# Optimization experiments

Measured on AMD Instinct MI355X. Metric: run time of the kernel, lower is better.

The kernel has to match this reference:

```python
import jax, jax.numpy as jnp
import numpy as np

D = 1024      # d_model
H = 16        # num_heads
HW = D // H   # head_width = 64
FF = 4 * D    # hidden_dim = 4096
BATCH = 2
T = 2048
EPS = 1e-5


def layer_norm(x, g, b):
    mu = jnp.mean(x, axis=-1, keepdims=True)
    var = jnp.mean(jnp.square(x - mu), axis=-1, keepdims=True)
    return (x - mu) * jax.lax.rsqrt(var + EPS) * g + b


def setup_inputs() -> dict:
    key = jax.random.key(0)
    ks = jax.random.split(key, 7)
    s = 0.02
    return {
        "x": jax.random.normal(ks[0], (BATCH, T, D), dtype=jnp.float32),
        "Wq": jax.random.normal(ks[1], (D, D), dtype=jnp.float32) * s,
        "Wk": jax.random.normal(ks[2], (D, D), dtype=jnp.float32) * s,
        "Wv": jax.random.normal(ks[3], (D, D), dtype=jnp.float32) * s,
        "W1": jax.random.normal(ks[4], (FF, D), dtype=jnp.float32) * s,
        "W2": jax.random.normal(ks[5], (D, FF), dtype=jnp.float32) * s,
        "g1": jnp.ones((D,), dtype=jnp.float32),
        "b1": jnp.zeros((D,), dtype=jnp.float32),
        "g2": jnp.ones((D,), dtype=jnp.float32),
        "b2": jnp.zeros((D,), dtype=jnp.float32),
    }


def reference(x, Wq, Wk, Wv, W1, W2, g1, b1, g2, b2):
    N, t, d = x.shape
    # norm1
    xn = layer_norm(x, g1, b1)

    # --- MHSA with ALiBi + causal mask (math mirrors torch module) ---
    def heads(y):  # (N,t,D) -> (N,H,t,HW)
        return y.reshape(N, t, H, HW).transpose(0, 2, 1, 3)

    q = heads(xn @ Wq.T)
    k = heads(xn @ Wk.T)
    v = heads(xn @ Wv.T)

    scores = jnp.einsum("nhqd,nhkd->nhqk", q, k) / np.sqrt(HW).astype(np.float32)

    pos = jnp.arange(t)
    rel = (pos[None, :] - pos[:, None]).astype(x.dtype)           # [t,t], rel[i,j]=j-i
    slopes = (2.0 ** (-(jnp.arange(1, H + 1)) * (8.0 / H))).astype(x.dtype)  # [H]
    alibi = slopes[:, None, None] * rel                            # [H,t,t]
    causal = jnp.where(pos[None, :] > pos[:, None],
                       jnp.array(-jnp.inf, x.dtype),
                       jnp.array(0.0, x.dtype))                    # [t,t]

    att = jax.nn.softmax(scores + alibi[None] + causal[None, None], axis=-1)
    o = jnp.einsum("nhqk,nhkd->nhqd", att, v)
    o = o.transpose(0, 2, 1, 3).reshape(N, t, d)

    att_out = xn + o

    # --- MLP: Linear -> SiLU -> Linear ---
    h = layer_norm(att_out, g2, b2)
    m = jax.nn.silu(h @ W1.T) @ W2.T
    return att_out + m
```

## Files before the change

### kernel.cpp

```cpp
#include <hip/hip_runtime.h>

#define DMODEL 1024
#define NHEAD  16
#define HWID   64
#define FFDIM  4096
#define NBATCH 2
#define SEQT   2048
#define NTOK   4096
#define QKLD   3072

using bf8    = __attribute__((ext_vector_type(8))) short;
using f32x4  = __attribute__((ext_vector_type(4))) float;
using f32x16 = __attribute__((ext_vector_type(16))) float;

__device__ inline short to_bf16(float f) {
  unsigned u = __float_as_uint(f);
  return (short)((u + 0x7fffu + ((u >> 16) & 1u)) >> 16);
}
__device__ inline float from_bf16(short s) {
  return __uint_as_float(((unsigned)(unsigned short)s) << 16);
}
__device__ inline float exp2_fast(float x) {
  float r;
  asm("v_exp_f32 %0, %1" : "=v"(r) : "v"(x));
  return r;
}
__device__ inline unsigned cvt_pk_bf16(float lo, float hi) {
  unsigned r;
  asm("v_cvt_pk_bf16_f32 %0, %1, %2" : "=v"(r) : "v"(lo), "v"(hi));
  return r;
}
__device__ inline void lds_load16(const void* g, void* l) {
  __builtin_amdgcn_global_load_lds(
      (const __attribute__((address_space(1))) void*)g,
      (__attribute__((address_space(3))) void*)l, 16, 0, 0);
}

__global__ __launch_bounds__(256)
void cvt_kernel(const float* __restrict__ in, short* __restrict__ out, int n4) {
  int i = blockIdx.x * 256 + threadIdx.x;
  if (i < n4) {
    float4 v = ((const float4*)in)[i];
    short4 o;
    o.x = to_bf16(v.x); o.y = to_bf16(v.y);
    o.z = to_bf16(v.z); o.w = to_bf16(v.w);
    ((short4*)out)[i] = o;
  }
}

__global__ __launch_bounds__(256)
void ln_kernel(const float* __restrict__ x, const float* __restrict__ g,
               const float* __restrict__ b, short* __restrict__ out) {
  const int row = blockIdx.x;
  const int t = threadIdx.x;
  const float4 v = ((const float4*)(x + (long)row * DMODEL))[t];
  float s  = v.x + v.y + v.z + v.w;
  float s2 = v.x * v.x + v.y * v.y + v.z * v.z + v.w * v.w;
#pragma unroll
  for (int m = 1; m < 64; m <<= 1) {
    s  += __shfl_xor(s, m);
    s2 += __shfl_xor(s2, m);
  }
  __shared__ float red[8];
  if ((t & 63) == 0) { red[t >> 6] = s; red[4 + (t >> 6)] = s2; }
  __syncthreads();
  s  = red[0] + red[1] + red[2] + red[3];
  s2 = red[4] + red[5] + red[6] + red[7];
  const float mu = s * (1.f / DMODEL);
  const float rs = rsqrtf(s2 * (1.f / DMODEL) - mu * mu + 1e-5f);
  const float4 gv = ((const float4*)g)[t];
  const float4 bv = ((const float4*)b)[t];
  short4 o;
  o.x = to_bf16((v.x - mu) * rs * gv.x + bv.x);
  o.y = to_bf16((v.y - mu) * rs * gv.y + bv.y);
  o.z = to_bf16((v.z - mu) * rs * gv.z + bv.z);
  o.w = to_bf16((v.w - mu) * rs * gv.w + bv.w);
  ((short4*)(out + (long)row * DMODEL))[t] = o;
}

template <int EPI>
__global__ __launch_bounds__(256, 3)
void gemm4(const short* __restrict__ A, const short* __restrict__ Bw,
           void* __restrict__ Cout, int N, int lda, int ldb, int K) {
  __shared__ short lds[3][2][4096];
  const int tid = threadIdx.x;
  const int w = tid >> 6, lane = tid & 63;
  const int l15 = lane & 15, l4 = lane >> 4;
  const int wr = (w >> 1) * 64, wc = (w & 1) * 64;

  const int gx = gridDim.x, nwg = gx * gridDim.y;
  const int wg = blockIdx.y * gx + blockIdx.x;
  const int sw = (wg & 7) * (nwg >> 3) + (wg >> 3);
  const int sx = gx >> 2;
  const int st = sw >> 4, w16 = sw & 15;
  const long bm = (long)((st / sx) * 4 + (w16 >> 2)) * 128;
  const long bn = (long)((st % sx) * 4 + (w16 & 3)) * 128;

  long aoff[2], boff[2];
#pragma unroll
  for (int i = 0; i < 2; ++i) {
    const int c = i * 4 + w;
    const int row = c * 16 + (lane >> 2);
    const int slog = (lane & 3) ^ ((row >> 1) & 3);
    aoff[i] = (bm + row) * (long)lda + slog * 8;
    boff[i] = (bn + row) * (long)ldb + slog * 8;
  }
  int offA[4], offB[4];
#pragma unroll
  for (int m = 0; m < 4; ++m) {
    const int row = wr + m * 16 + l15;
    offA[m] = row * 64 + ((l4 ^ ((row >> 1) & 3)) << 4);
  }
#pragma unroll
  for (int n = 0; n < 4; ++n) {
    const int row = wc + n * 16 + l15;
    offB[n] = row * 64 + ((l4 ^ ((row >> 1) & 3)) << 4);
  }

  const int NT = K >> 5;
  f32x4 acc[4][4] = {};

#pragma unroll
  for (int t = 0; t < 2; ++t) {
    char* db = (char*)&lds[t][0][0];
#pragma unroll
    for (int i = 0; i < 2; ++i) {
      const int c = i * 4 + w;
      lds_load16(A  + aoff[i] + t * 32, db + c * 1024);
      lds_load16(Bw + boff[i] + t * 32, db + 8192 + c * 1024);
    }
  }

  int slot = 0, pslot = 2;
  for (int t = 0; t < NT; ++t) {
    if (t + 1 < NT) asm volatile("s_waitcnt vmcnt(4)" ::: "memory");
    else            asm volatile("s_waitcnt vmcnt(0)" ::: "memory");
    __builtin_amdgcn_s_barrier();
    asm volatile("" ::: "memory");
    if (t + 2 < NT) {
      char* db = (char*)&lds[pslot][0][0];
      const long ks = (long)(t + 2) * 32;
#pragma unroll
      for (int i = 0; i < 2; ++i) {
        const int c = i * 4 + w;
        lds_load16(A  + aoff[i] + ks, db + c * 1024);
        lds_load16(Bw + boff[i] + ks, db + 8192 + c * 1024);
      }
    }
    const char* sb = (const char*)&lds[slot][0][0];
    bf8 af[4], bfr[4];
#pragma unroll
    for (int m = 0; m < 4; ++m) af[m] = *(const bf8*)(sb + offA[m]);
#pragma unroll
    for (int n = 0; n < 4; ++n) bfr[n] = *(const bf8*)(sb + 8192 + offB[n]);
    __builtin_amdgcn_s_setprio(1);
#pragma unroll
    for (int m = 0; m < 4; ++m)
#pragma unroll
      for (int n = 0; n < 4; ++n)
        acc[m][n] = __builtin_amdgcn_mfma_f32_16x16x32_bf16(af[m], bfr[n], acc[m][n], 0, 0, 0);
    __builtin_amdgcn_s_setprio(0);
    slot  = (slot  == 2) ? 0 : slot  + 1;
    pslot = (pslot == 2) ? 0 : pslot + 1;
  }

#pragma unroll
  for (int m = 0; m < 4; ++m)
#pragma unroll
    for (int n = 0; n < 4; ++n) {
      const long col = bn + wc + n * 16 + l15;
#pragma unroll
      for (int r = 0; r < 4; ++r) {
        const long row = bm + wr + m * 16 + l4 * 4 + r;
        float v = acc[m][n][r];
        if (EPI == 0) {
          ((short*)Cout)[row * N + col] = to_bf16(v);
        } else if (EPI == 1) {
          ((short*)Cout)[row * N + col] = to_bf16(v / (1.f + __expf(-v)));
        } else {
          float* Cp = (float*)Cout;
          const long idx = row * N + col;
          Cp[idx] = Cp[idx] + v;
        }
      }
    }
}

__global__ __launch_bounds__(256)
void pack_k(const short* __restrict__ qkv, short* __restrict__ Kp) {
  const int g = blockIdx.x, bh = blockIdx.y;
  const int b = bh >> 4, h = bh & 15;
  const int t = threadIdx.x;
  const int row = t >> 3, cc = t & 7, c = cc >> 1, hi = cc & 1;
  const bf8 v = *(const bf8*)&qkv[(long)(b * SEQT + g * 32 + row) * QKLD +
                                  1024 + h * HWID + c * 16 + hi * 8];
  *(bf8*)&Kp[(((long)bh * 256 + g * 4 + c) * 64 + hi * 32 + row) * 8] = v;
}

__global__ __launch_bounds__(256)
void pack_v(const short* __restrict__ qkv, short* __restrict__ Vp) {
  __shared__ short tile[64][72];
  const int tc = blockIdx.x, bh = blockIdx.y;
  const int b = bh >> 4, h = bh & 15;
  const int t = threadIdx.x;
  {
    const int r = t >> 2, c = (t & 3) * 16;
    const long src = (long)(b * SEQT + tc * 64 + r) * QKLD + 2048 + h * HWID + c;
    *(bf8*)&tile[r][c]     = *(const bf8*)&qkv[src];
    *(bf8*)&tile[r][c + 8] = *(const bf8*)&qkv[src + 8];
  }
  __syncthreads();
  const int dg = t >> 7, ch = (t >> 5) & 3, row = t & 31;
#pragma unroll
  for (int hi = 0; hi < 2; ++hi) {
    short o[8];
#pragma unroll
    for (int j = 0; j < 8; ++j) o[j] = tile[ch * 16 + hi * 8 + j][dg * 32 + row];
    *(bf8*)&Vp[(((long)bh * 256 + dg * 128 + tc * 4 + ch) * 64 + hi * 32 + row) * 8] =
        *(bf8*)o;
  }
}

__global__ __launch_bounds__(64, 2)
void attn_kernel(const short* __restrict__ qkv, const short* __restrict__ Kp,
                 const short* __restrict__ Vp, const short* __restrict__ xn,
                 float* __restrict__ att) {
  const int L = blockIdx.x;
  const int bh = (L & 7) * 4 + ((L >> 3) & 3);
  const int qtile = 63 - (L >> 5);
  const int b = bh >> 4, h = bh & 15;
  const int q0 = qtile * 32;
  const int lane = threadIdx.x;
  const int l31 = lane & 31, hi = lane >> 5;
  const long tokbase = (long)b * SEQT;

  bf8 qf[4];
  {
    const short* qrow = qkv + (tokbase + q0 + l31) * QKLD + h * HWID + hi * 8;
#pragma unroll
    for (int c = 0; c < 4; ++c) qf[c] = *(const bf8*)(qrow + c * 16);
  }

  const float slope2 = exp2f(-0.5f * (float)(h + 1)) * 1.44269504f;
  const float sc2 = 0.125f * 1.44269504f;
  float arr[16];
#pragma unroll
  for (int r = 0; r < 16; ++r) arr[r] = slope2 * (float)((r & 3) + 8 * (r >> 2));
  const float hofs = slope2 * 4.f * (float)hi;
  const float qabs = (float)(q0 + l31);

  float m2 = -1e30f, lsum = 0.f;
  f32x16 acc0 = {}, acc1 = {};
  const int ktm = q0 >> 6;
  const bf8* kfb = (const bf8*)Kp + (long)bh * 16384 + lane;
  const bf8* vfb = (const bf8*)Vp + (long)bh * 16384 + lane;

  bf8 kc[8], kn[8], vc[8];
#pragma unroll
  for (int c = 0; c < 4; ++c) {
    kc[c]     = kfb[c * 64];
    kc[4 + c] = kfb[256 + c * 64];
  }

#pragma unroll 2
  for (int kt = 0; kt <= ktm; ++kt) {
    const int k0 = kt * 64;
    const long vb = (long)kt * 256;
#pragma unroll
    for (int ch = 0; ch < 4; ++ch) {
      vc[ch]     = vfb[vb + ch * 64];
      vc[4 + ch] = vfb[8192 + vb + ch * 64];
    }
    const long nb = (long)(kt < ktm ? kt + 1 : kt) * 512;
#pragma unroll
    for (int c = 0; c < 4; ++c) {
      kn[c]     = kfb[nb + c * 64];
      kn[4 + c] = kfb[nb + 256 + c * 64];
    }
    f32x16 s0 = {}, s1 = {};
#pragma unroll
    for (int c = 0; c < 4; ++c) {
      s0 = __builtin_amdgcn_mfma_f32_32x32x16_bf16(kc[c], qf[c], s0, 0, 0, 0);
      s1 = __builtin_amdgcn_mfma_f32_32x32x16_bf16(kc[4 + c], qf[c], s1, 0, 0, 0);
    }
    const float base = slope2 * ((float)k0 - qabs) + hofs;
    float s[32];
#pragma unroll
    for (int r = 0; r < 16; ++r) {
      s[r]      = fmaf(s0[r], sc2, base + arr[r]);
      s[16 + r] = fmaf(s1[r], sc2, base + arr[r] + slope2 * 32.f);
    }
    if (kt == ktm) {
      const int qi = q0 + l31;
#pragma unroll
      for (int r = 0; r < 16; ++r) {
        const int krel = (r & 3) + 8 * (r >> 2) + 4 * hi;
        if (k0 + krel > qi)      s[r]      = -1e30f;
        if (k0 + 32 + krel > qi) s[16 + r] = -1e30f;
      }
    }
    float ma = s[0], mb = s[1], mc = s[2], md = s[3];
#pragma unroll
    for (int i = 4; i < 32; i += 4) {
      ma = fmaxf(ma, s[i]); mb = fmaxf(mb, s[i + 1]);
      mc = fmaxf(mc, s[i + 2]); md = fmaxf(md, s[i + 3]);
    }
    float pm = fmaxf(fmaxf(ma, mb), fmaxf(mc, md));
    pm = fmaxf(pm, __shfl_xor(pm, 32));
    if (!__all(pm - m2 <= 11.0f)) {
      const float nm = fmaxf(m2, pm);
      const float alpha = exp2_fast(m2 - nm);
      m2 = nm;
      lsum *= alpha;
      acc0 *= alpha;
      acc1 *= alpha;
    }
    float p[32];
#pragma unroll
    for (int i = 0; i < 32; ++i) p[i] = exp2_fast(s[i] - m2);
    float sa = p[0], sb = p[1], sc = p[2], sd = p[3];
#pragma unroll
    for (int i = 4; i < 32; i += 4) {
      sa += p[i]; sb += p[i + 1]; sc += p[i + 2]; sd += p[i + 3];
    }
    float rs = (sa + sb) + (sc + sd);
    rs += __shfl_xor(rs, 32);
    lsum += rs;
    unsigned cpk[16];
#pragma unroll
    for (int g = 0; g < 8; ++g) {
      cpk[g]     = cvt_pk_bf16(p[2 * g], p[2 * g + 1]);
      cpk[8 + g] = cvt_pk_bf16(p[16 + 2 * g], p[16 + 2 * g + 1]);
    }
    bf8 pb[4];
#pragma unroll
    for (int ch = 0; ch < 4; ++ch) {
      const int cb = (ch >> 1) * 8 + (ch & 1) * 4;
      unsigned u0 = cpk[cb + 0], u2 = cpk[cb + 2];
      unsigned u1 = cpk[cb + 1], u3 = cpk[cb + 3];
      asm("v_permlane32_swap_b32 %0, %1" : "+v"(u0), "+v"(u2));
      asm("v_permlane32_swap_b32 %0, %1" : "+v"(u1), "+v"(u3));
      union { unsigned u[4]; bf8 v; } f;
      f.u[0] = u0; f.u[1] = u1; f.u[2] = u2; f.u[3] = u3;
      pb[ch] = f.v;
    }
#pragma unroll
    for (int ch = 0; ch < 4; ++ch) {
      acc0 = __builtin_amdgcn_mfma_f32_32x32x16_bf16(vc[ch], pb[ch], acc0, 0, 0, 0);
      acc1 = __builtin_amdgcn_mfma_f32_32x32x16_bf16(vc[4 + ch], pb[ch], acc1, 0, 0, 0);
    }
#pragma unroll
    for (int i = 0; i < 8; ++i) kc[i] = kn[i];
  }

  __shared__ float Os[32 * 68];
  const float rl = 1.f / lsum;
#pragma unroll
  for (int r = 0; r < 16; ++r) {
    const int d0 = (r & 3) + 8 * (r >> 2) + 4 * hi;
    Os[l31 * 68 + d0]      = acc0[r] * rl;
    Os[l31 * 68 + 32 + d0] = acc1[r] * rl;
  }
  __syncthreads();
#pragma unroll
  for (int it = 0; it < 8; ++it) {
    const int idx = it * 64 + lane;
    const int row = idx >> 4, c4 = idx & 15;
    const float4 ov = *(const float4*)&Os[row * 68 + c4 * 4];
    const long gbase = (tokbase + q0 + row) * DMODEL + h * HWID + c4 * 4;
    const short4 xv = *(const short4*)&xn[gbase];
    float4 o;
    o.x = ov.x + from_bf16(xv.x);
    o.y = ov.y + from_bf16(xv.y);
    o.z = ov.z + from_bf16(xv.z);
    o.w = ov.w + from_bf16(xv.w);
    *(float4*)&att[gbase] = o;
  }
}

extern "C" void kernel_launch(void* const* d_in, const int* in_sizes, int n_in,
                              void* d_out, int out_size, void* d_ws, size_t ws_size,
                              hipStream_t stream) {
  (void)in_sizes; (void)n_in; (void)out_size; (void)ws_size;
  const float* x  = (const float*)d_in[0];
  const float* Wq = (const float*)d_in[1];
  const float* Wk = (const float*)d_in[2];
  const float* Wv = (const float*)d_in[3];
  const float* W1 = (const float*)d_in[4];
  const float* W2 = (const float*)d_in[5];
  const float* g1 = (const float*)d_in[6];
  const float* b1 = (const float*)d_in[7];
  const float* g2 = (const float*)d_in[8];
  const float* b2 = (const float*)d_in[9];

  char* ws = (char*)d_ws;
  const size_t MB = 1024 * 1024;
  short* wqkv_b = (short*)(ws + 0);
  short* w1_b   = (short*)(ws + 6  * MB);
  short* w2_b   = (short*)(ws + 14 * MB);
  short* xn     = (short*)(ws + 22 * MB);
  short* qkv    = (short*)(ws + 30 * MB);
  short* m1     = (short*)(ws + 22 * MB);
  short* Kp     = (short*)(ws + 54 * MB);
  short* Vp     = (short*)(ws + 62 * MB);
  short* hb     = (short*)(ws + 70 * MB);
  float* att    = (float*)d_out;

  cvt_kernel<<<1024, 256, 0, stream>>>(Wq, wqkv_b, 262144);
  cvt_kernel<<<1024, 256, 0, stream>>>(Wk, wqkv_b + 1048576, 262144);
  cvt_kernel<<<1024, 256, 0, stream>>>(Wv, wqkv_b + 2097152, 262144);
  cvt_kernel<<<4096, 256, 0, stream>>>(W1, w1_b, 1048576);
  cvt_kernel<<<4096, 256, 0, stream>>>(W2, w2_b, 1048576);

  ln_kernel<<<NTOK, 256, 0, stream>>>(x, g1, b1, xn);

  gemm4<0><<<dim3(24, 32), 256, 0, stream>>>(xn, wqkv_b, qkv, QKLD, DMODEL, DMODEL, DMODEL);
  pack_k<<<dim3(64, 32), 256, 0, stream>>>(qkv, Kp);
  pack_v<<<dim3(32, 32), 256, 0, stream>>>(qkv, Vp);

  attn_kernel<<<2048, 64, 0, stream>>>(qkv, Kp, Vp, xn, att);

  ln_kernel<<<NTOK, 256, 0, stream>>>(att, g2, b2, hb);

  gemm4<1><<<dim3(32, 32), 256, 0, stream>>>(hb, w1_b, m1, FFDIM, DMODEL, DMODEL, DMODEL);
  gemm4<2><<<dim3(8, 32), 256, 0, stream>>>(m1, w2_b, d_out, DMODEL, FFDIM, FFDIM, FFDIM);
}
```

Before: 218.9 us.

## Split-K the second MLP GEMM with atomics and merge small launch kernels

Result: slower. 232.2 us (+6.1%).

```diff
diff --git a/kernel.cpp b/kernel.cpp
--- a/kernel.cpp
+++ b/kernel.cpp
@@ -37,15 +37,23 @@
 }
 
 __global__ __launch_bounds__(256)
-void cvt_kernel(const float* __restrict__ in, short* __restrict__ out, int n4) {
+void cvt_all(const float* __restrict__ Wq, const float* __restrict__ Wk,
+             const float* __restrict__ Wv, const float* __restrict__ W1,
+             const float* __restrict__ W2, short* __restrict__ wqkv,
+             short* __restrict__ w1b, short* __restrict__ w2b) {
   int i = blockIdx.x * 256 + threadIdx.x;
-  if (i < n4) {
-    float4 v = ((const float4*)in)[i];
-    short4 o;
-    o.x = to_bf16(v.x); o.y = to_bf16(v.y);
-    o.z = to_bf16(v.z); o.w = to_bf16(v.w);
-    ((short4*)out)[i] = o;
-  }
+  const float* src;
+  short* dst;
+  if (i < 1048576)      { src = W1; dst = w1b; }
+  else if (i < 2097152) { src = W2; dst = w2b;            i -= 1048576; }
+  else if (i < 2359296) { src = Wq; dst = wqkv;           i -= 2097152; }
+  else if (i < 2621440) { src = Wk; dst = wqkv + 1048576; i -= 2359296; }
+  else                  { src = Wv; dst = wqkv + 2097152; i -= 2621440; }
+  float4 v = ((const float4*)src)[i];
+  short4 o;
+  o.x = to_bf16(v.x); o.y = to_bf16(v.y);
+  o.z = to_bf16(v.z); o.w = to_bf16(v.w);
+  ((short4*)dst)[i] = o;
 }
 
 __global__ __launch_bounds__(256)
@@ -81,7 +89,7 @@
 template <int EPI>
 __global__ __launch_bounds__(256, 3)
 void gemm4(const short* __restrict__ A, const short* __restrict__ Bw,
-           void* __restrict__ Cout, int N, int lda, int ldb, int K) {
+           void* __restrict__ Cout, int N, int lda, int ldb, int Kslice) {
   __shared__ short lds[3][2][4096];
   const int tid = threadIdx.x;
   const int w = tid >> 6, lane = tid & 63;
@@ -95,6 +103,7 @@
   const int st = sw >> 4, w16 = sw & 15;
   const long bm = (long)((st / sx) * 4 + (w16 >> 2)) * 128;
   const long bn = (long)((st % sx) * 4 + (w16 & 3)) * 128;
+  const long kofs = (long)blockIdx.z * Kslice;
 
   long aoff[2], boff[2];
 #pragma unroll
@@ -102,8 +111,8 @@
     const int c = i * 4 + w;
     const int row = c * 16 + (lane >> 2);
     const int slog = (lane & 3) ^ ((row >> 1) & 3);
-    aoff[i] = (bm + row) * (long)lda + slog * 8;
-    boff[i] = (bn + row) * (long)ldb + slog * 8;
+    aoff[i] = (bm + row) * (long)lda + slog * 8 + kofs;
+    boff[i] = (bn + row) * (long)ldb + slog * 8 + kofs;
   }
   int offA[4], offB[4];
 #pragma unroll
@@ -117,7 +126,7 @@
     offB[n] = row * 64 + ((l4 ^ ((row >> 1) & 3)) << 4);
   }
 
-  const int NT = K >> 5;
+  const int NT = Kslice >> 5;
   f32x4 acc[4][4] = {};
 
 #pragma unroll
@@ -178,46 +187,43 @@
         } else if (EPI == 1) {
           ((short*)Cout)[row * N + col] = to_bf16(v / (1.f + __expf(-v)));
         } else {
-          float* Cp = (float*)Cout;
-          const long idx = row * N + col;
-          Cp[idx] = Cp[idx] + v;
+          atomicAdd(&((float*)Cout)[row * N + col], v);
         }
       }
     }
 }
 
 __global__ __launch_bounds__(256)
-void pack_k(const short* __restrict__ qkv, short* __restrict__ Kp) {
-  const int g = blockIdx.x, bh = blockIdx.y;
+void pack_kv(const short* __restrict__ qkv, short* __restrict__ Kp,
+             short* __restrict__ Vp) {
+  __shared__ short tile[64][72];
+  const int bx = blockIdx.x, bh = blockIdx.y;
   const int b = bh >> 4, h = bh & 15;
   const int t = threadIdx.x;
-  const int row = t >> 3, cc = t & 7, c = cc >> 1, hi = cc & 1;
-  const bf8 v = *(const bf8*)&qkv[(long)(b * SEQT + g * 32 + row) * QKLD +
-                                  1024 + h * HWID + c * 16 + hi * 8];
-  *(bf8*)&Kp[(((long)bh * 256 + g * 4 + c) * 64 + hi * 32 + row) * 8] = v;
-}
-
-__global__ __launch_bounds__(256)
-void pack_v(const short* __restrict__ qkv, short* __restrict__ Vp) {
-  __shared__ short tile[64][72];
-  const int tc = blockIdx.x, bh = blockIdx.y;
-  const int b = bh >> 4, h = bh & 15;
-  const int t = threadIdx.x;
-  {
-    const int r = t >> 2, c = (t & 3) * 16;
-    const long src = (long)(b * SEQT + tc * 64 + r) * QKLD + 2048 + h * HWID + c;
-    *(bf8*)&tile[r][c]     = *(const bf8*)&qkv[src];
-    *(bf8*)&tile[r][c + 8] = *(const bf8*)&qkv[src + 8];
-  }
-  __syncthreads();
-  const int dg = t >> 7, ch = (t >> 5) & 3, row = t & 31;
-#pragma unroll
-  for (int hi = 0; hi < 2; ++hi) {
-    short o[8];
-#pragma unroll
-    for (int j = 0; j < 8; ++j) o[j] = tile[ch * 16 + hi * 8 + j][dg * 32 + row];
-    *(bf8*)&Vp[(((long)bh * 256 + dg * 128 + tc * 4 + ch) * 64 + hi * 32 + row) * 8] =
-        *(bf8*)o;
+  if (bx < 64) {
+    const int g = bx;
+    const int row = t >> 3, cc = t & 7, c = cc >> 1, hi = cc & 1;
+    const bf8 v = *(const bf8*)&qkv[(long)(b * SEQT + g * 32 + row) * QKLD +
+                                    1024 + h * HWID + c * 16 + hi * 8];
+    *(bf8*)&Kp[(((long)bh * 256 + g * 4 + c) * 64 + hi * 32 + row) * 8] = v;
+  } else {
+    const int tc = bx - 64;
+    {
+      const int r = t >> 2, c = (t & 3) * 16;
+      const long src = (long)(b * SEQT + tc * 64 + r) * QKLD + 2048 + h * HWID + c;
+      *(bf8*)&tile[r][c]     = *(const bf8*)&qkv[src];
+      *(bf8*)&tile[r][c + 8] = *(const bf8*)&qkv[src + 8];
+    }
+    __syncthreads();
+    const int dg = t >> 7, ch = (t >> 5) & 3, row = t & 31;
+#pragma unroll
+    for (int hi = 0; hi < 2; ++hi) {
+      short o[8];
+#pragma unroll
+      for (int j = 0; j < 8; ++j) o[j] = tile[ch * 16 + hi * 8 + j][dg * 32 + row];
+      *(bf8*)&Vp[(((long)bh * 256 + dg * 128 + tc * 4 + ch) * 64 + hi * 32 + row) * 8] =
+          *(bf8*)o;
+    }
   }
 }
 
@@ -406,22 +412,17 @@
   short* hb     = (short*)(ws + 70 * MB);
   float* att    = (float*)d_out;
 
-  cvt_kernel<<<1024, 256, 0, stream>>>(Wq, wqkv_b, 262144);
-  cvt_kernel<<<1024, 256, 0, stream>>>(Wk, wqkv_b + 1048576, 262144);
-  cvt_kernel<<<1024, 256, 0, stream>>>(Wv, wqkv_b + 2097152, 262144);
-  cvt_kernel<<<4096, 256, 0, stream>>>(W1, w1_b, 1048576);
-  cvt_kernel<<<4096, 256, 0, stream>>>(W2, w2_b, 1048576);
+  cvt_all<<<11264, 256, 0, stream>>>(Wq, Wk, Wv, W1, W2, wqkv_b, w1_b, w2_b);
 
   ln_kernel<<<NTOK, 256, 0, stream>>>(x, g1, b1, xn);
 
   gemm4<0><<<dim3(24, 32), 256, 0, stream>>>(xn, wqkv_b, qkv, QKLD, DMODEL, DMODEL, DMODEL);
-  pack_k<<<dim3(64, 32), 256, 0, stream>>>(qkv, Kp);
-  pack_v<<<dim3(32, 32), 256, 0, stream>>>(qkv, Vp);
+  pack_kv<<<dim3(96, 32), 256, 0, stream>>>(qkv, Kp, Vp);
 
   attn_kernel<<<2048, 64, 0, stream>>>(qkv, Kp, Vp, xn, att);
 
   ln_kernel<<<NTOK, 256, 0, stream>>>(att, g2, b2, hb);
 
   gemm4<1><<<dim3(32, 32), 256, 0, stream>>>(hb, w1_b, m1, FFDIM, DMODEL, DMODEL, DMODEL);
-  gemm4<2><<<dim3(8, 32), 256, 0, stream>>>(m1, w2_b, d_out, DMODEL, FFDIM, FFDIM, FFDIM);
-}
+  gemm4<3><<<dim3(8, 32, 4), 256, 0, stream>>>(m1, w2_b, d_out, DMODEL, FFDIM, FFDIM, 1024);
+}
```
